# Performance work log

Hardware: AMD Instinct MI355X
Metric: run time of the kernel (lower is better)

## Reference

```python
import jax, jax.numpy as jnp
import numpy as np
import math

B, S, D, H, FF = 2, 2048, 1024, 16, 4096
HD = D // H
EPS = 1e-5


def setup_inputs() -> dict:
    key = jax.random.key(0)
    ks = jax.random.split(key, 16)
    w = lambda k, shape: (jax.random.normal(k, shape, jnp.float32) * 0.02)
    future = jnp.triu(jnp.ones((S, S), dtype=bool), k=1)
    causal_mask = jnp.where(future, -jnp.inf, 0.0).astype(jnp.float32)
    return {
        "src": jax.random.normal(ks[0], (B, S, D), jnp.float32),
        "causal_mask": causal_mask,
        "Wq": w(ks[1], (D, D)), "bq": jnp.zeros((D,), jnp.float32),
        "Wk": w(ks[2], (D, D)), "bk": jnp.zeros((D,), jnp.float32),
        "Wv": w(ks[3], (D, D)), "bv": jnp.zeros((D,), jnp.float32),
        "Wo": w(ks[4], (D, D)), "bo": jnp.zeros((D,), jnp.float32),
        "W1": w(ks[5], (D, FF)), "b1": jnp.zeros((FF,), jnp.float32),
        "W2": w(ks[6], (FF, D)), "b2": jnp.zeros((D,), jnp.float32),
        "ln1_g": jnp.ones((D,), jnp.float32), "ln1_b": jnp.zeros((D,), jnp.float32),
        "ln2_g": jnp.ones((D,), jnp.float32), "ln2_b": jnp.zeros((D,), jnp.float32),
    }


def _layernorm(x, g, b):
    mu = jnp.mean(x, axis=-1, keepdims=True)
    var = jnp.mean((x - mu) ** 2, axis=-1, keepdims=True)
    return (x - mu) * jax.lax.rsqrt(var + EPS) * g + b


def reference(src, causal_mask, Wq, bq, Wk, bk, Wv, bv, Wo, bo,
              W1, b1, W2, b2, ln1_g, ln1_b, ln2_g, ln2_b):
    # QKV projections, split heads: [B,S,D] -> [B,H,S,HD]
    def split_heads(x):
        return x.reshape(B, S, H, HD).transpose(0, 2, 1, 3)

    q = split_heads(src @ Wq + bq)
    k = split_heads(src @ Wk + bk)
    v = split_heads(src @ Wv + bv)

    # scores: [B,H,S,S]; attn_mask = causal_mask broadcast over batch, then head dim
    scores = jnp.einsum("bhqd,bhkd->bhqk", q, k) / math.sqrt(HD)
    scores = scores + causal_mask[None, None, :, :]
    # scores[scores != scores] = 0
    scores = jnp.where(jnp.isnan(scores), 0.0, scores)
    # rows that are entirely inf -> 0
    mask_all_inf = jnp.all(jnp.isinf(scores), axis=-1, keepdims=True)
    scores = jnp.where(mask_all_inf, 0.0, scores)
    attn = jax.nn.softmax(scores, axis=-1)
    attn = jnp.where(jnp.isnan(attn), 0.0, attn)

    ctx = jnp.einsum("bhqk,bhkd->bhqd", attn, v)
    ctx = ctx.transpose(0, 2, 1, 3).reshape(B, S, D)
    attn_out = ctx @ Wo + bo

    x = _layernorm(src + attn_out, ln1_g, ln1_b)
    ff = jax.nn.relu(x @ W1 + b1) @ W2 + b2
    return _layernorm(x + ff, ln2_g, ln2_b)
```

## Files before the change

### kernel.cpp

```cpp
#include <hip/hip_runtime.h>

#define SS 2048
#define DD 1024
#define HH 16
#define HDIM 64
#define BB 2
#define FFD 4096
#define MR (BB*SS)
#define QKVLD 3072

typedef __bf16 bf16;
typedef __bf16 bf16x4 __attribute__((ext_vector_type(4)));
typedef __bf16 bf16x8 __attribute__((ext_vector_type(8)));
typedef float f32x4 __attribute__((ext_vector_type(4)));

struct P4 { bf16* p[4]; };
struct TP4 { const float* src[4]; bf16* dst[4]; float scale[4]; };

__device__ inline f32x4 mfma32(bf16x8 a, bf16x8 b, f32x4 c) {
  return __builtin_amdgcn_mfma_f32_16x16x32_bf16(a, b, c, 0, 0, 0);
}

__device__ inline void gload_lds16(const void* g, void* l) {
  __builtin_amdgcn_global_load_lds(
      (const __attribute__((address_space(1))) void*)g,
      (__attribute__((address_space(3))) void*)l, 16, 0, 0);
}

#if defined(__has_builtin)
#if __has_builtin(__builtin_amdgcn_exp2f)
#define HAVE_EXP2_BUILTIN 1
#endif
#endif
__device__ inline float fast_exp2(float x) {
#ifdef HAVE_EXP2_BUILTIN
  return __builtin_amdgcn_exp2f(x);
#else
  float r; asm("v_exp_f32 %0, %1" : "=v"(r) : "v"(x)); return r;
#endif
}

__global__ __launch_bounds__(256)
void cvt_bf16_kernel(const float* __restrict__ in, bf16* __restrict__ out, int n) {
  int i = (blockIdx.x * 256 + threadIdx.x) * 4;
  if (i >= n) return;
  float4 v = *(const float4*)(in + i);
  bf16x4 o;
  o[0] = (bf16)v.x; o[1] = (bf16)v.y; o[2] = (bf16)v.z; o[3] = (bf16)v.w;
  *(bf16x4*)(out + i) = o;
}

__global__ __launch_bounds__(256)
void concat_bias_kernel(const float* __restrict__ bq, const float* __restrict__ bk,
                        const float* __restrict__ bv, float* __restrict__ out) {
  int i = blockIdx.x * 256 + threadIdx.x;
  const float K2 = 0.18033688f;
  out[i] = i < 1024 ? bq[i] * K2 : (i < 2048 ? bk[i - 1024] : bv[i - 2048]);
}

__global__ __launch_bounds__(256)
void transpose_w4_kernel(TP4 t) {
  __shared__ float tl[32][33];
  const float* W = t.src[blockIdx.z];
  bf16* Wt = t.dst[blockIdx.z];
  const float sc = t.scale[blockIdx.z];
  int tx = threadIdx.x & 31, ty = threadIdx.x >> 5;
  int n0 = blockIdx.x * 32, k0 = blockIdx.y * 32;
  #pragma unroll
  for (int i = 0; i < 4; ++i)
    tl[ty + i*8][tx] = W[(size_t)(k0 + ty + i*8) * DD + n0 + tx];
  __syncthreads();
  #pragma unroll
  for (int i = 0; i < 4; ++i)
    Wt[(size_t)(n0 + ty + i*8) * DD + k0 + tx] = (bf16)(tl[tx][ty + i*8] * sc);
}

__global__ __launch_bounds__(256)
void transpose_w_kernel(const float* __restrict__ W, bf16* __restrict__ Wt,
                        int K, int N) {
  __shared__ float t[32][33];
  int tx = threadIdx.x & 31, ty = threadIdx.x >> 5;
  int n0 = blockIdx.x * 32, k0 = blockIdx.y * 32;
  #pragma unroll
  for (int i = 0; i < 4; ++i)
    t[ty + i*8][tx] = W[(size_t)(k0 + ty + i*8) * N + n0 + tx];
  __syncthreads();
  #pragma unroll
  for (int i = 0; i < 4; ++i)
    Wt[(size_t)(n0 + ty + i*8) * K + k0 + tx] = (bf16)t[tx][ty + i*8];
}

__global__ __launch_bounds__(256)
void transpose_v_kernel(const bf16* __restrict__ V2d, bf16* __restrict__ Vt) {
  __shared__ bf16 t[32][33];
  int tx = threadIdx.x & 31, ty = threadIdx.x >> 5;
  int s0 = blockIdx.x * 32, d0 = blockIdx.y * 32;
  int bh = blockIdx.z;
  int b = bh >> 4, h = bh & 15;
  #pragma unroll
  for (int i = 0; i < 4; ++i)
    t[ty + i*8][tx] = V2d[(size_t)(b*SS + s0 + ty + i*8) * QKVLD + h*HDIM + d0 + tx];
  __syncthreads();
  #pragma unroll
  for (int i = 0; i < 4; ++i)
    Vt[((size_t)bh*HDIM + d0 + ty + i*8) * SS + s0 + tx] = t[tx][ty + i*8];
}

template<int OUT_BF16, int RELU, int SPLITK>
__global__ __launch_bounds__(512)
void gemm256(const bf16* __restrict__ A, const bf16* __restrict__ Bt,
             const float* __restrict__ bias, void* __restrict__ Cout,
             P4 part, int Ndim, int Kdim) {
  __shared__ bf16 Asm[3][256 * 64];
  __shared__ bf16 Bsm[2][256 * 64];
  const int gx = gridDim.x, gy = gridDim.y;
  const int gxy = gx * gy;
  const int nwg = gxy * gridDim.z;
  const int lin = (blockIdx.z * gy + blockIdx.y) * gx + blockIdx.x;
  const int swz = (lin & 7) * (nwg >> 3) + (lin >> 3);
  int bz = 0, rem = swz;
  if (SPLITK > 1) { bz = swz / gxy; rem = swz - bz * gxy; }
  const int by = rem / gx, bx = rem - by * gx;
  const int m0 = by * 256, n0 = bx * 256;
  const int tid = threadIdx.x;
  const int wave = tid >> 6, lane = tid & 63;
  const int g = lane >> 4, r = lane & 15;
  const int wr = wave >> 2, wn = wave & 3;
  const int kstart = bz * (Kdim / SPLITK);

  const int srow = wave * 8 + (lane >> 3);
  const int skslot = (lane & 7) ^ (lane >> 3);
  const bf16* Ag = A + (size_t)(m0 + srow) * Kdim + kstart + skslot * 8;
  const bf16* Bg = Bt + (size_t)(n0 + srow) * Kdim + kstart + skslot * 8;

  f32x4 acc[8][4] = {};
  const int NT = (Kdim / SPLITK) >> 6;

  auto stageA = [&](int t) {
    if (t >= NT) return;
    const int kb = t << 6;
    bf16* Ad = Asm[t % 3];
    #pragma unroll
    for (int j = 0; j < 4; ++j)
      gload_lds16(Ag + (size_t)j * 64 * Kdim + kb, Ad + (j * 64 + wave * 8) * 64);
  };
  auto stageB = [&](int t) {
    if (t >= NT) return;
    const int kb = t << 6;
    bf16* Bd = Bsm[t & 1];
    #pragma unroll
    for (int j = 0; j < 4; ++j)
      gload_lds16(Bg + (size_t)j * 64 * Kdim + kb, Bd + (j * 64 + wave * 8) * 64);
  };

  stageA(0);
  stageB(0);
  stageA(1);
  asm volatile("s_waitcnt vmcnt(4)" ::: "memory");
  asm volatile("s_barrier" ::: "memory");

  for (int t = 0; t < NT; ++t) {
    const bf16* Ab = Asm[t % 3];
    const bf16* Bb = Bsm[t & 1];
    bf16x8 bfr[4][2];
    #pragma unroll
    for (int i = 0; i < 4; ++i) {
      const int rowb = wn * 64 + i * 16 + r;
      #pragma unroll
      for (int kk = 0; kk < 2; ++kk)
        bfr[i][kk] = *(const bf16x8*)(Bb + rowb * 64 + (((kk * 4 + g) ^ (r & 7)) * 8));
    }
    #pragma unroll
    for (int ph = 0; ph < 2; ++ph) {
      bf16x8 af[4][2];
      #pragma unroll
      for (int i = 0; i < 4; ++i) {
        const int row = wr * 128 + (ph * 4 + i) * 16 + r;
        #pragma unroll
        for (int kk = 0; kk < 2; ++kk)
          af[i][kk] = *(const bf16x8*)(Ab + row * 64 + (((kk * 4 + g) ^ (r & 7)) * 8));
      }
      if (ph == 0) stageB(t + 1);
      if (ph == 1) stageA(t + 2);
      asm volatile("s_barrier" ::: "memory");
      __builtin_amdgcn_s_setprio(1);
      #pragma unroll
      for (int i = 0; i < 4; ++i)
        #pragma unroll
        for (int jn = 0; jn < 4; ++jn)
          #pragma unroll
          for (int kk = 0; kk < 2; ++kk)
            acc[ph * 4 + i][jn] = mfma32(af[i][kk], bfr[jn][kk], acc[ph * 4 + i][jn]);
      __builtin_amdgcn_s_setprio(0);
      asm volatile("s_barrier" ::: "memory");
    }
    if (t + 1 < NT) {
      if (t + 2 < NT) asm volatile("s_waitcnt vmcnt(4)" ::: "memory");
      else            asm volatile("s_waitcnt vmcnt(0)" ::: "memory");
      asm volatile("s_barrier" ::: "memory");
    }
  }

  #pragma unroll
  for (int mi = 0; mi < 8; ++mi) {
    #pragma unroll
    for (int ni = 0; ni < 4; ++ni) {
      const int col = n0 + wn * 64 + ni * 16 + r;
      const float bv = (SPLITK > 1) ? 0.f : bias[col];
      #pragma unroll
      for (int jj = 0; jj < 4; ++jj) {
        const int row = m0 + wr * 128 + mi * 16 + g * 4 + jj;
        float v = acc[mi][ni][jj] + bv;
        if (RELU) v = fmaxf(v, 0.f);
        if (SPLITK > 1) part.p[bz][(size_t)row * Ndim + col] = (bf16)v;
        else if (OUT_BF16) ((bf16*)Cout)[(size_t)row * Ndim + col] = (bf16)v;
        else               ((float*)Cout)[(size_t)row * Ndim + col] = v;
      }
    }
  }
}

__global__ __launch_bounds__(256)
void attn_kernel(const bf16* __restrict__ Q2d, const bf16* __restrict__ K2d,
                 const bf16* __restrict__ Vt, bf16* __restrict__ ctx) {
  __shared__ bf16 Ks[2 * 4096];
  __shared__ bf16 Vs[2 * 4096];
  const int tid = threadIdx.x;
  const int wave = tid >> 6;
  const int lane = tid & 63;
  const int g = lane >> 4, r = lane & 15;
  const int lin = blockIdx.y * gridDim.x + blockIdx.x;
  const int swz = (lin & 7) * 64 + (lin >> 3);
  const int p = swz & 15;
  const int bh = swz >> 4;
  const int b = bh >> 4, h = bh & 15;

  const int strow = wave * 16 + (lane >> 2);
  const int lslot = (lane & 3) ^ ((lane >> 3) & 3);
  const bf16* srcK0 = K2d + (size_t)(b*SS + strow) * QKVLD + h*HDIM + lslot * 8;
  const bf16* srcK1 = srcK0 + 32;
  const bf16* srcV0 = Vt + ((size_t)bh*HDIM + strow) * SS + lslot * 8;
  const bf16* srcV1 = srcV0 + 32;

  auto sw = [](int row, int s) { return row * 32 + ((s ^ ((row >> 1) & 3)) * 8); };

  const int kr0 = 8 * (r >> 2) + (r & 3);
  const int oKa0 = sw(kr0,      g), oKb0 = 2048 + oKa0;
  const int oKa1 = sw(kr0 +  4, g), oKb1 = 2048 + oKa1;
  const int oKa2 = sw(kr0 + 32, g), oKb2 = 2048 + oKa2;
  const int oKa3 = sw(kr0 + 36, g), oKb3 = 2048 + oKa3;
  int oV[4];
  #pragma unroll
  for (int c = 0; c < 4; ++c) oV[c] = sw(c * 16 + r, g);

  bf16x8 onesf;
  #pragma unroll
  for (int j = 0; j < 8; ++j) onesf[j] = (bf16)1.0f;

  #pragma unroll
  for (int tt = 0; tt < 2; ++tt) {
    const int tile = tt ? (31 - p) : p;
    const int q0 = tile * 64 + wave * 16;
    const int qg = q0 + r;
    const bf16* qp = Q2d + (size_t)(b*SS + q0 + r) * QKVLD + h * HDIM;
    const bf16x8 qf0 = *(const bf16x8*)(qp + g * 8);
    const bf16x8 qf1 = *(const bf16x8*)(qp + 32 + g * 8);
    f32x4 ov[4] = {};
    f32x4 lacc = {};
    const int nst = tile + 1;
    {
      bf16* kb = Ks + wave * 512;
      bf16* vb = Vs + wave * 512;
      gload_lds16(srcK0, kb);
      gload_lds16(srcK1, kb + 2048);
      gload_lds16(srcV0, vb);
      gload_lds16(srcV1, vb + 2048);
    }
    __syncthreads();
    int cur = 0;
    for (int st = 0; st < nst; ++st) {
      const int k0 = st * 64;
      if (st + 1 < nst) {
        const int kn = k0 + 64;
        bf16* kb = Ks + (cur ^ 1) * 4096 + wave * 512;
        bf16* vb = Vs + (cur ^ 1) * 4096 + wave * 512;
        gload_lds16(srcK0 + (size_t)kn * QKVLD, kb);
        gload_lds16(srcK1 + (size_t)kn * QKVLD, kb + 2048);
        gload_lds16(srcV0 + kn, vb);
        gload_lds16(srcV1 + kn, vb + 2048);
      }
      const bf16* Kb = Ks + cur * 4096;
      const bf16* Vb = Vs + cur * 4096;
      f32x4 c0 = {}, c1 = {}, c2 = {}, c3 = {};
      __builtin_amdgcn_s_setprio(1);
      c0 = mfma32(*(const bf16x8*)(Kb + oKa0), qf0, c0);
      c1 = mfma32(*(const bf16x8*)(Kb + oKa1), qf0, c1);
      c2 = mfma32(*(const bf16x8*)(Kb + oKa2), qf0, c2);
      c3 = mfma32(*(const bf16x8*)(Kb + oKa3), qf0, c3);
      c0 = mfma32(*(const bf16x8*)(Kb + oKb0), qf1, c0);
      c1 = mfma32(*(const bf16x8*)(Kb + oKb1), qf1, c1);
      c2 = mfma32(*(const bf16x8*)(Kb + oKb2), qf1, c2);
      c3 = mfma32(*(const bf16x8*)(Kb + oKb3), qf1, c3);
      __builtin_amdgcn_s_setprio(0);
      float p0[4], p1[4], p2[4], p3[4];
      const bool need_mask = (k0 + 63 > qg);
      #pragma unroll
      for (int j = 0; j < 4; ++j) {
        float s0 = c0[j];
        float s1 = c1[j];
        float s2 = c2[j];
        float s3 = c3[j];
        if (need_mask) {
          if (k0 + 8*g + j > qg)          s0 = -3.0e38f;
          if (k0 + 8*g + 4 + j > qg)      s1 = -3.0e38f;
          if (k0 + 32 + 8*g + j > qg)     s2 = -3.0e38f;
          if (k0 + 32 + 8*g + 4 + j > qg) s3 = -3.0e38f;
        }
        p0[j] = fast_exp2(s0);
        p1[j] = fast_exp2(s1);
        p2[j] = fast_exp2(s2);
        p3[j] = fast_exp2(s3);
      }
      bf16x8 pfa, pfb;
      #pragma unroll
      for (int j = 0; j < 4; ++j) {
        pfa[j] = (bf16)p0[j]; pfa[4 + j] = (bf16)p1[j];
        pfb[j] = (bf16)p2[j]; pfb[4 + j] = (bf16)p3[j];
      }
      __builtin_amdgcn_s_setprio(1);
      #pragma unroll
      for (int c = 0; c < 4; ++c) {
        bf16x8 vfa = *(const bf16x8*)(Vb + oV[c]);
        bf16x8 vfb = *(const bf16x8*)(Vb + 2048 + oV[c]);
        ov[c] = mfma32(pfa, vfa, ov[c]);
        ov[c] = mfma32(pfb, vfb, ov[c]);
      }
      lacc = mfma32(pfa, onesf, lacc);
      lacc = mfma32(pfb, onesf, lacc);
      __builtin_amdgcn_s_setprio(0);
      __syncthreads();
      cur ^= 1;
    }
    #pragma unroll
    for (int j = 0; j < 4; ++j) {
      const float inv = 1.f / lacc[j];
      const int row = b*SS + q0 + 4*g + j;
      #pragma unroll
      for (int c = 0; c < 4; ++c)
        ctx[(size_t)row * DD + h*HDIM + c*16 + r] = (bf16)(ov[c][j] * inv);
    }
  }
}

template<int WRITEB>
__global__ __launch_bounds__(256)
void ln_bf4_kernel(const float* __restrict__ a, P4 part, const float* __restrict__ cb,
                   const float* __restrict__ gam, const float* __restrict__ bet,
                   float* __restrict__ outf, bf16* __restrict__ outb) {
  const int row = blockIdx.x;
  const int tid = threadIdx.x;
  const size_t base = (size_t)row * DD + tid * 4;
  float4 va = *(const float4*)(a + base);
  bf16x4 u0 = *(const bf16x4*)(part.p[0] + base);
  bf16x4 u1 = *(const bf16x4*)(part.p[1] + base);
  bf16x4 u2 = *(const bf16x4*)(part.p[2] + base);
  bf16x4 u3 = *(const bf16x4*)(part.p[3] + base);
  float4 vb4 = *(const float4*)(cb + tid * 4);
  float x0 = va.x + ((float)u0[0] + (float)u1[0]) + ((float)u2[0] + (float)u3[0]) + vb4.x;
  float x1 = va.y + ((float)u0[1] + (float)u1[1]) + ((float)u2[1] + (float)u3[1]) + vb4.y;
  float x2 = va.z + ((float)u0[2] + (float)u1[2]) + ((float)u2[2] + (float)u3[2]) + vb4.z;
  float x3 = va.w + ((float)u0[3] + (float)u1[3]) + ((float)u2[3] + (float)u3[3]) + vb4.w;
  float s  = x0 + x1 + x2 + x3;
  float s2 = x0*x0 + x1*x1 + x2*x2 + x3*x3;
  #pragma unroll
  for (int off = 32; off > 0; off >>= 1) {
    s  += __shfl_xor(s,  off);
    s2 += __shfl_xor(s2, off);
  }
  __shared__ float red[8];
  const int wv = tid >> 6;
  if ((tid & 63) == 0) { red[wv] = s; red[wv + 4] = s2; }
  __syncthreads();
  s  = red[0] + red[1] + red[2] + red[3];
  s2 = red[4] + red[5] + red[6] + red[7];
  const float mu  = s * (1.f / DD);
  const float var = s2 * (1.f / DD) - mu * mu;
  const float rs  = rsqrtf(var + 1e-5f);
  float4 vg = *(const float4*)(gam + tid * 4);
  float4 vb = *(const float4*)(bet + tid * 4);
  float y0 = (x0 - mu) * rs * vg.x + vb.x;
  float y1 = (x1 - mu) * rs * vg.y + vb.y;
  float y2 = (x2 - mu) * rs * vg.z + vb.z;
  float y3 = (x3 - mu) * rs * vg.w + vb.w;
  float4 yo; yo.x = y0; yo.y = y1; yo.z = y2; yo.w = y3;
  *(float4*)(outf + base) = yo;
  if (WRITEB) {
    bf16x4 ob;
    ob[0] = (bf16)y0; ob[1] = (bf16)y1; ob[2] = (bf16)y2; ob[3] = (bf16)y3;
    *(bf16x4*)(outb + base) = ob;
  }
}

extern "C" void kernel_launch(void* const* d_in, const int* in_sizes, int n_in,
                              void* d_out, int out_size, void* d_ws, size_t ws_size,
                              hipStream_t stream) {
  const float* src  = (const float*)d_in[0];
  const float* Wq   = (const float*)d_in[2];
  const float* bq   = (const float*)d_in[3];
  const float* Wk   = (const float*)d_in[4];
  const float* bk   = (const float*)d_in[5];
  const float* Wv   = (const float*)d_in[6];
  const float* bv   = (const float*)d_in[7];
  const float* Wo   = (const float*)d_in[8];
  const float* bo   = (const float*)d_in[9];
  const float* W1   = (const float*)d_in[10];
  const float* b1   = (const float*)d_in[11];
  const float* W2   = (const float*)d_in[12];
  const float* b2   = (const float*)d_in[13];
  const float* ln1g = (const float*)d_in[14];
  const float* ln1b = (const float*)d_in[15];
  const float* ln2g = (const float*)d_in[16];
  const float* ln2b = (const float*)d_in[17];

  char* ws = (char*)d_ws;
  const size_t MB = 1024 * 1024;
  bf16* wqkvt = (bf16*)(ws + 0 * MB);
  bf16* wot   = (bf16*)(ws + 6 * MB);
  bf16* w1t   = (bf16*)(ws + 8 * MB);
  bf16* w2t   = (bf16*)(ws + 16 * MB);
  bf16* bsrc  = (bf16*)(ws + 24 * MB);
  bf16* xb    = bsrc;
  bf16* qkv   = (bf16*)(ws + 32 * MB);
  bf16* vt    = (bf16*)(ws + 56 * MB);
  bf16* ctx   = (bf16*)(ws + 64 * MB);
  bf16* ff1   = qkv;
  float* xf   = (float*)(ws + 72 * MB);
  float* bqkv = (float*)(ws + 88 * MB);
  float* outp = (float*)d_out;

  P4 wop;
  wop.p[0] = (bf16*)(ws + 32 * MB);
  wop.p[1] = (bf16*)(ws + 40 * MB);
  wop.p[2] = (bf16*)(ws + 48 * MB);
  wop.p[3] = (bf16*)(ws + 56 * MB);
  P4 fp;
  fp.p[0] = (bf16*)(ws + 0 * MB);
  fp.p[1] = (bf16*)(ws + 8 * MB);
  fp.p[2] = (bf16*)(ws + 24 * MB);
  fp.p[3] = (bf16*)(ws + 64 * MB);

  cvt_bf16_kernel<<<(MR * DD) / 1024, 256, 0, stream>>>(src, bsrc, MR * DD);
  TP4 tp;
  tp.src[0] = Wq; tp.dst[0] = wqkvt;              tp.scale[0] = 0.18033688f;
  tp.src[1] = Wk; tp.dst[1] = wqkvt + 1024*1024;  tp.scale[1] = 1.f;
  tp.src[2] = Wv; tp.dst[2] = wqkvt + 2048*1024;  tp.scale[2] = 1.f;
  tp.src[3] = Wo; tp.dst[3] = wot;                tp.scale[3] = 1.f;
  transpose_w4_kernel<<<dim3(32, 32, 4), 256, 0, stream>>>(tp);
  transpose_w_kernel<<<dim3(128, 32), 256, 0, stream>>>(W1, w1t, DD, FFD);
  transpose_w_kernel<<<dim3(32, 128), 256, 0, stream>>>(W2, w2t, FFD, DD);
  concat_bias_kernel<<<12, 256, 0, stream>>>(bq, bk, bv, bqkv);

  gemm256<1, 0, 1><<<dim3(QKVLD / 256, MR / 256), 512, 0, stream>>>(bsrc, wqkvt, bqkv, qkv, P4{}, QKVLD, DD);
  transpose_v_kernel<<<dim3(SS / 32, HDIM / 32, BB * HH), 256, 0, stream>>>(qkv + 2048, vt);

  attn_kernel<<<dim3(16, BB * HH), 256, 0, stream>>>(qkv, qkv + 1024, vt, ctx);

  gemm256<0, 0, 4><<<dim3(DD / 256, MR / 256, 4), 512, 0, stream>>>(ctx, wot, nullptr, nullptr, wop, DD, DD);
  ln_bf4_kernel<1><<<MR, 256, 0, stream>>>(src, wop, bo, ln1g, ln1b, xf, xb);

  gemm256<1, 1, 1><<<dim3(FFD / 256, MR / 256), 512, 0, stream>>>(xb, w1t, b1, ff1, P4{}, FFD, DD);
  gemm256<0, 0, 4><<<dim3(DD / 256, MR / 256, 4), 512, 0, stream>>>(ff1, w2t, nullptr, nullptr, fp, DD, FFD);
  ln_bf4_kernel<0><<<MR, 256, 0, stream>>>(xf, fp, b2, ln2g, ln2b, outp, nullptr);
}
```

Baseline: 221.0 us.

## Add 128x256 GEMM kernel with K32 double buffering for QKV and FFN1

Adds a new GEMM kernel with 128x256 output tiles, K-step 32 and two-stage LDS double buffering via direct global-to-LDS loads. It is used for the QKV projection and the first FFN projection in place of the 256x256 kernel. Halving the M tile doubles the workgroup count, which is meant to fill more of the GPU's compute units on these mid-sized GEMMs. In exchange each tile reuses operands less, and the shallower pipeline with a barrier every 32 K-elements may expose more memory latency.

```diff
diff --git a/kernel.cpp b/kernel.cpp
--- a/kernel.cpp
+++ b/kernel.cpp
@@ -104,6 +104,88 @@
   #pragma unroll
   for (int i = 0; i < 4; ++i)
     Vt[((size_t)bh*HDIM + d0 + ty + i*8) * SS + s0 + tx] = t[tx][ty + i*8];
+}
+
+template<int OUT_BF16, int RELU>
+__global__ __launch_bounds__(512)
+void gemm_h(const bf16* __restrict__ A, const bf16* __restrict__ Bt,
+            const float* __restrict__ bias, void* __restrict__ Cout,
+            int Ndim, int Kdim) {
+  __shared__ bf16 Asm[2][128 * 32];
+  __shared__ bf16 Bsm[2][256 * 32];
+  const int gx = gridDim.x;
+  const int nwg = gx * gridDim.y;
+  const int lin = blockIdx.y * gx + blockIdx.x;
+  const int swz = (lin & 7) * (nwg >> 3) + (lin >> 3);
+  const int by = swz / gx, bx = swz - by * gx;
+  const int m0 = by * 128, n0 = bx * 256;
+  const int tid = threadIdx.x;
+  const int wave = tid >> 6, lane = tid & 63;
+  const int g = lane >> 4, r = lane & 15;
+  const int wr = wave >> 2, wn = wave & 3;
+
+  const int lrow = lane >> 2;
+  const int lslot = (lane & 3) ^ (lrow & 3);
+  const bf16* Ag = A + (size_t)(m0 + wave * 16 + lrow) * Kdim + lslot * 8;
+  const bf16* Bg0 = Bt + (size_t)(n0 + wave * 32 + lrow) * Kdim + lslot * 8;
+  const bf16* Bg1 = Bg0 + (size_t)16 * Kdim;
+
+  f32x4 acc[4][4] = {};
+  const int NT = Kdim >> 5;
+
+  auto stage = [&](int t) {
+    const int kb = t << 5;
+    bf16* Ad = Asm[t & 1] + wave * 512;
+    bf16* Bd = Bsm[t & 1] + wave * 1024;
+    gload_lds16(Ag + kb, Ad);
+    gload_lds16(Bg0 + kb, Bd);
+    gload_lds16(Bg1 + kb, Bd + 512);
+  };
+
+  stage(0);
+  __syncthreads();
+
+  for (int t = 0; t < NT; ++t) {
+    const bf16* Ab = Asm[t & 1];
+    const bf16* Bb = Bsm[t & 1];
+    bf16x8 af[4], bfr[4];
+    #pragma unroll
+    for (int i = 0; i < 4; ++i) {
+      const int row = wr * 64 + i * 16 + r;
+      af[i] = *(const bf16x8*)(Ab + row * 32 + ((g ^ (r & 3)) * 8));
+    }
+    #pragma unroll
+    for (int i = 0; i < 4; ++i) {
+      const int rowb = wn * 64 + i * 16 + r;
+      bfr[i] = *(const bf16x8*)(Bb + rowb * 32 + ((g ^ (r & 3)) * 8));
+    }
+    if (t + 1 < NT) stage(t + 1);
+    __builtin_amdgcn_s_setprio(1);
+    #pragma unroll
+    for (int i = 0; i < 4; ++i)
+      #pragma unroll
+      for (int jn = 0; jn < 4; ++jn)
+        acc[i][jn] = mfma32(af[i], bfr[jn], acc[i][jn]);
+    __builtin_amdgcn_s_setprio(0);
+    __syncthreads();
+  }
+
+  #pragma unroll
+  for (int mi = 0; mi < 4; ++mi) {
+    #pragma unroll
+    for (int ni = 0; ni < 4; ++ni) {
+      const int col = n0 + wn * 64 + ni * 16 + r;
+      const float bv = bias[col];
+      #pragma unroll
+      for (int jj = 0; jj < 4; ++jj) {
+        const int row = m0 + wr * 64 + mi * 16 + g * 4 + jj;
+        float v = acc[mi][ni][jj] + bv;
+        if (RELU) v = fmaxf(v, 0.f);
+        if (OUT_BF16) ((bf16*)Cout)[(size_t)row * Ndim + col] = (bf16)v;
+        else          ((float*)Cout)[(size_t)row * Ndim + col] = v;
+      }
+    }
+  }
 }
 
 template<int OUT_BF16, int RELU, int SPLITK>
@@ -460,7 +542,7 @@
   transpose_w_kernel<<<dim3(32, 128), 256, 0, stream>>>(W2, w2t, FFD, DD);
   concat_bias_kernel<<<12, 256, 0, stream>>>(bq, bk, bv, bqkv);
 
-  gemm256<1, 0, 1><<<dim3(QKVLD / 256, MR / 256), 512, 0, stream>>>(bsrc, wqkvt, bqkv, qkv, P4{}, QKVLD, DD);
+  gemm_h<1, 0><<<dim3(QKVLD / 256, MR / 128), 512, 0, stream>>>(bsrc, wqkvt, bqkv, qkv, QKVLD, DD);
   transpose_v_kernel<<<dim3(SS / 32, HDIM / 32, BB * HH), 256, 0, stream>>>(qkv + 2048, vt);
 
   attn_kernel<<<dim3(16, BB * HH), 256, 0, stream>>>(qkv, qkv + 1024, vt, ctx);
@@ -468,7 +550,7 @@
   gemm256<0, 0, 4><<<dim3(DD / 256, MR / 256, 4), 512, 0, stream>>>(ctx, wot, nullptr, nullptr, wop, DD, DD);
   ln_bf4_kernel<1><<<MR, 256, 0, stream>>>(src, wop, bo, ln1g, ln1b, xf, xb);
 
-  gemm256<1, 1, 1><<<dim3(FFD / 256, MR / 256), 512, 0, stream>>>(xb, w1t, b1, ff1, P4{}, FFD, DD);
+  gemm_h<1, 1><<<dim3(FFD / 256, MR / 128), 512, 0, stream>>>(xb, w1t, b1, ff1, FFD, DD);
   gemm256<0, 0, 4><<<dim3(DD / 256, MR / 256, 4), 512, 0, stream>>>(ff1, w2t, nullptr, nullptr, fp, DD, FFD);
   ln_bf4_kernel<0><<<MR, 256, 0, stream>>>(xf, fp, b2, ln2g, ln2b, outp, nullptr);
 }
```

Measured after the change: 218.5 us. Within noise of the previous version (-1.1%).

## Replace 256x256 GEMM with smaller 128x256 tile, K=32 double-buffered kernel

Applied to the files above, without the earlier changes.

Replaces the 256x256-tile GEMM, which used a triple-buffered A and K-step of 64, with a 128x256 tile, K-step of 32, simple double buffering and __syncthreads per step. Each wave now computes a 64x64 sub-tile with half the accumulators. The aim is to launch more workgroups, cut LDS and register pressure, and improve occupancy and load balance across CUs. In exchange, operand reuse per tile is lower and a block barrier runs every 32-wide K step, which may expose more global-load latency.

```diff
diff --git a/kernel.cpp b/kernel.cpp
--- a/kernel.cpp
+++ b/kernel.cpp
@@ -108,11 +108,11 @@
 
 template<int OUT_BF16, int RELU, int SPLITK>
 __global__ __launch_bounds__(512)
-void gemm256(const bf16* __restrict__ A, const bf16* __restrict__ Bt,
-             const float* __restrict__ bias, void* __restrict__ Cout,
-             P4 part, int Ndim, int Kdim) {
-  __shared__ bf16 Asm[3][256 * 64];
-  __shared__ bf16 Bsm[2][256 * 64];
+void gemm_h(const bf16* __restrict__ A, const bf16* __restrict__ Bt,
+            const float* __restrict__ bias, void* __restrict__ Cout,
+            P4 part, int Ndim, int Kdim) {
+  __shared__ bf16 Asm[2][128 * 32];
+  __shared__ bf16 Bsm[2][256 * 32];
   const int gx = gridDim.x, gy = gridDim.y;
   const int gxy = gx * gy;
   const int nwg = gxy * gridDim.z;
@@ -121,95 +121,68 @@
   int bz = 0, rem = swz;
   if (SPLITK > 1) { bz = swz / gxy; rem = swz - bz * gxy; }
   const int by = rem / gx, bx = rem - by * gx;
-  const int m0 = by * 256, n0 = bx * 256;
+  const int m0 = by * 128, n0 = bx * 256;
   const int tid = threadIdx.x;
   const int wave = tid >> 6, lane = tid & 63;
   const int g = lane >> 4, r = lane & 15;
   const int wr = wave >> 2, wn = wave & 3;
   const int kstart = bz * (Kdim / SPLITK);
 
-  const int srow = wave * 8 + (lane >> 3);
-  const int skslot = (lane & 7) ^ (lane >> 3);
-  const bf16* Ag = A + (size_t)(m0 + srow) * Kdim + kstart + skslot * 8;
-  const bf16* Bg = Bt + (size_t)(n0 + srow) * Kdim + kstart + skslot * 8;
-
-  f32x4 acc[8][4] = {};
-  const int NT = (Kdim / SPLITK) >> 6;
-
-  auto stageA = [&](int t) {
-    if (t >= NT) return;
-    const int kb = t << 6;
-    bf16* Ad = Asm[t % 3];
+  const int lrow = lane >> 2;
+  const int lslot = (lane & 3) ^ (lrow & 3);
+  const bf16* Ag = A + (size_t)(m0 + wave * 16 + lrow) * Kdim + kstart + lslot * 8;
+  const bf16* Bg0 = Bt + (size_t)(n0 + wave * 32 + lrow) * Kdim + kstart + lslot * 8;
+  const bf16* Bg1 = Bg0 + (size_t)16 * Kdim;
+
+  f32x4 acc[4][4] = {};
+  const int NT = (Kdim / SPLITK) >> 5;
+
+  auto stage = [&](int t) {
+    const int kb = t << 5;
+    bf16* Ad = Asm[t & 1] + wave * 512;
+    bf16* Bd = Bsm[t & 1] + wave * 1024;
+    gload_lds16(Ag + kb, Ad);
+    gload_lds16(Bg0 + kb, Bd);
+    gload_lds16(Bg1 + kb, Bd + 512);
+  };
+
+  stage(0);
+  __syncthreads();
+
+  for (int t = 0; t < NT; ++t) {
+    const bf16* Ab = Asm[t & 1];
+    const bf16* Bb = Bsm[t & 1];
+    bf16x8 af[4], bfr[4];
     #pragma unroll
-    for (int j = 0; j < 4; ++j)
-      gload_lds16(Ag + (size_t)j * 64 * Kdim + kb, Ad + (j * 64 + wave * 8) * 64);
-  };
-  auto stageB = [&](int t) {
-    if (t >= NT) return;
-    const int kb = t << 6;
-    bf16* Bd = Bsm[t & 1];
-    #pragma unroll
-    for (int j = 0; j < 4; ++j)
-      gload_lds16(Bg + (size_t)j * 64 * Kdim + kb, Bd + (j * 64 + wave * 8) * 64);
-  };
-
-  stageA(0);
-  stageB(0);
-  stageA(1);
-  asm volatile("s_waitcnt vmcnt(4)" ::: "memory");
-  asm volatile("s_barrier" ::: "memory");
-
-  for (int t = 0; t < NT; ++t) {
-    const bf16* Ab = Asm[t % 3];
-    const bf16* Bb = Bsm[t & 1];
-    bf16x8 bfr[4][2];
+    for (int i = 0; i < 4; ++i) {
+      const int row = wr * 64 + i * 16 + r;
+      af[i] = *(const bf16x8*)(Ab + row * 32 + ((g ^ (r & 3)) * 8));
+    }
     #pragma unroll
     for (int i = 0; i < 4; ++i) {
       const int rowb = wn * 64 + i * 16 + r;
-      #pragma unroll
-      for (int kk = 0; kk < 2; ++kk)
-        bfr[i][kk] = *(const bf16x8*)(Bb + rowb * 64 + (((kk * 4 + g) ^ (r & 7)) * 8));
-    }
+      bfr[i] = *(const bf16x8*)(Bb + rowb * 32 + ((g ^ (r & 3)) * 8));
+    }
+    if (t + 1 < NT) stage(t + 1);
+    __builtin_amdgcn_s_setprio(1);
     #pragma unroll
-    for (int ph = 0; ph < 2; ++ph) {
-      bf16x8 af[4][2];
-      #pragma unroll
-      for (int i = 0; i < 4; ++i) {
-        const int row = wr * 128 + (ph * 4 + i) * 16 + r;
-        #pragma unroll
-        for (int kk = 0; kk < 2; ++kk)
-          af[i][kk] = *(const bf16x8*)(Ab + row * 64 + (((kk * 4 + g) ^ (r & 7)) * 8));
-      }
-      if (ph == 0) stageB(t + 1);
-      if (ph == 1) stageA(t + 2);
-      asm volatile("s_barrier" ::: "memory");
-      __builtin_amdgcn_s_setprio(1);
-      #pragma unroll
-      for (int i = 0; i < 4; ++i)
-        #pragma unroll
-        for (int jn = 0; jn < 4; ++jn)
-          #pragma unroll
-          for (int kk = 0; kk < 2; ++kk)
-            acc[ph * 4 + i][jn] = mfma32(af[i][kk], bfr[jn][kk], acc[ph * 4 + i][jn]);
-      __builtin_amdgcn_s_setprio(0);
-      asm volatile("s_barrier" ::: "memory");
-    }
-    if (t + 1 < NT) {
-      if (t + 2 < NT) asm volatile("s_waitcnt vmcnt(4)" ::: "memory");
-      else            asm volatile("s_waitcnt vmcnt(0)" ::: "memory");
-      asm volatile("s_barrier" ::: "memory");
-    }
+    for (int i = 0; i < 4; ++i)
+      #pragma unroll
+      for (int jn = 0; jn < 4; ++jn)
+        acc[i][jn] = mfma32(af[i], bfr[jn], acc[i][jn]);
+    __builtin_amdgcn_s_setprio(0);
+    __syncthreads();
   }
 
   #pragma unroll
-  for (int mi = 0; mi < 8; ++mi) {
+  for (int mi = 0; mi < 4; ++mi) {
     #pragma unroll
     for (int ni = 0; ni < 4; ++ni) {
       const int col = n0 + wn * 64 + ni * 16 + r;
       const float bv = (SPLITK > 1) ? 0.f : bias[col];
       #pragma unroll
       for (int jj = 0; jj < 4; ++jj) {
-        const int row = m0 + wr * 128 + mi * 16 + g * 4 + jj;
+        const int row = m0 + wr * 64 + mi * 16 + g * 4 + jj;
         float v = acc[mi][ni][jj] + bv;
         if (RELU) v = fmaxf(v, 0.f);
         if (SPLITK > 1) part.p[bz][(size_t)row * Ndim + col] = (bf16)v;
@@ -460,15 +433,15 @@
   transpose_w_kernel<<<dim3(32, 128), 256, 0, stream>>>(W2, w2t, FFD, DD);
   concat_bias_kernel<<<12, 256, 0, stream>>>(bq, bk, bv, bqkv);
 
-  gemm256<1, 0, 1><<<dim3(QKVLD / 256, MR / 256), 512, 0, stream>>>(bsrc, wqkvt, bqkv, qkv, P4{}, QKVLD, DD);
+  gemm_h<1, 0, 1><<<dim3(QKVLD / 256, MR / 128), 512, 0, stream>>>(bsrc, wqkvt, bqkv, qkv, P4{}, QKVLD, DD);
   transpose_v_kernel<<<dim3(SS / 32, HDIM / 32, BB * HH), 256, 0, stream>>>(qkv + 2048, vt);
 
   attn_kernel<<<dim3(16, BB * HH), 256, 0, stream>>>(qkv, qkv + 1024, vt, ctx);
 
-  gemm256<0, 0, 4><<<dim3(DD / 256, MR / 256, 4), 512, 0, stream>>>(ctx, wot, nullptr, nullptr, wop, DD, DD);
+  gemm_h<0, 0, 4><<<dim3(DD / 256, MR / 128, 4), 512, 0, stream>>>(ctx, wot, nullptr, nullptr, wop, DD, DD);
   ln_bf4_kernel<1><<<MR, 256, 0, stream>>>(src, wop, bo, ln1g, ln1b, xf, xb);
 
-  gemm256<1, 1, 1><<<dim3(FFD / 256, MR / 256), 512, 0, stream>>>(xb, w1t, b1, ff1, P4{}, FFD, DD);
-  gemm256<0, 0, 4><<<dim3(DD / 256, MR / 256, 4), 512, 0, stream>>>(ff1, w2t, nullptr, nullptr, fp, DD, FFD);
+  gemm_h<1, 1, 1><<<dim3(FFD / 256, MR / 128), 512, 0, stream>>>(xb, w1t, b1, ff1, P4{}, FFD, DD);
+  gemm_h<0, 0, 4><<<dim3(DD / 256, MR / 128, 4), 512, 0, stream>>>(ff1, w2t, nullptr, nullptr, fp, DD, FFD);
   ln_bf4_kernel<0><<<MR, 256, 0, stream>>>(xf, fp, b2, ln2g, ln2b, outp, nullptr);
 }
```

New measurement: 219.8 us. No clear change (-0.6%).
